# Kernel optimization log

Hardware: AMD Instinct MI355X
Metric: run time of the kernel (lower is better)

Reference implementation:

```python
import jax, jax.numpy as jnp
import numpy as np

N = 32768      # nodes
DIN = 256      # in_channels (space dim; hyperbolic input has DIN+1 dims)
DOUT = 256     # out_channels
H = 8          # num_heads
K = 1.0        # Lorentz curvature manifold.k
P = 2          # power_k
EPS = 1e-6


def _lorentz(key, n, d):
    # random point on Lorentz manifold: time = sqrt(||space||^2 + k)
    s = jax.random.normal(key, (n, d), jnp.float32)
    t = jnp.sqrt(jnp.sum(s * s, -1, keepdims=True) + K)
    return jnp.concatenate([t, s], -1)


def setup_inputs() -> dict:
    key = jax.random.key(0)
    ks = jax.random.split(key, 8)
    sc = 0.02
    return {
        "query_input": _lorentz(ks[0], N, DIN),
        "source_input": _lorentz(ks[1], N, DIN),
        "Wq_w": jax.random.normal(ks[2], (H, DOUT, DIN + 1), jnp.float32) * sc,
        "Wq_b": jnp.zeros((H, DOUT), jnp.float32),
        "Wk_w": jax.random.normal(ks[3], (H, DOUT, DIN + 1), jnp.float32) * sc,
        "Wk_b": jnp.zeros((H, DOUT), jnp.float32),
        "Wv_w": jax.random.normal(ks[4], (H, DOUT, DIN + 1), jnp.float32) * sc,
        "Wv_b": jnp.zeros((H, DOUT), jnp.float32),
        "norm_scale": jnp.ones((), jnp.float32),
        "v_map_w": jax.random.normal(ks[5], (DOUT, DIN), jnp.float32) * sc,
        "v_map_b": jnp.zeros((DOUT,), jnp.float32),
        "final_w": jax.random.normal(ks[6], (DOUT, H * DOUT), jnp.float32) * sc,
        "final_b": jnp.zeros((DOUT,), jnp.float32),
    }


def _hyp_linear(x, W, b):
    # HypLinear for all heads at once. x: [N, Din+1], W: [H, Dout, Din+1], b: [H, Dout]
    xs = jnp.einsum('ni,hoi->nho', x, W) + b              # space part [N,H,Dout]
    xt = jnp.sqrt(jnp.sum(xs * xs, -1, keepdims=True) + K)  # Lorentz time
    return jnp.concatenate([xt, xs], -1)                  # [N,H,Dout+1]


def _fp(x, p=P):
    # fp(x) = ||x|| / ||x^p|| * x^p  (per-vector rescaled power map)
    norm_x = jnp.linalg.norm(x, axis=-1, keepdims=True)
    xp = x ** p
    norm_xp = jnp.linalg.norm(xp, axis=-1, keepdims=True)
    return norm_x / norm_xp * xp


def reference(query_input, source_input, Wq_w, Wq_b, Wk_w, Wk_b, Wv_w, Wv_b,
              norm_scale, v_map_w, v_map_b, final_w, final_b):
    q = _hyp_linear(query_input, Wq_w, Wq_b)    # [N,H,D+1]
    k = _hyp_linear(source_input, Wk_w, Wk_b)   # [N,H,D+1]
    v = _hyp_linear(source_input, Wv_w, Wv_b)   # [N,H,D+1]

    # linear_focus_attention: drop time dim
    qs, ks_, vs = q[..., 1:], k[..., 1:], v[..., 1:]     # [N,H,D]
    dscale = jnp.abs(norm_scale) + EPS
    phi_q = _fp((jax.nn.relu(qs) + EPS) / dscale)
    phi_k = _fp((jax.nn.relu(ks_) + EPS) / dscale)

    ktv = jnp.einsum('nhm,nhd->hmd', phi_k, vs)          # [H,D,D]
    numerator = jnp.einsum('nhm,hmd->nhd', phi_q, ktv)   # [N,H,D]
    denominator = jnp.einsum('nhd,hd->nh', phi_q, jnp.sum(phi_k, 0))[..., None]
    attn = numerator / (denominator + EPS)

    vss = vs @ v_map_w.T + v_map_b                       # v_map_mlp(v)
    attn = attn + vss

    # trans_heads_concat -> final_linear
    out = attn.reshape(N, H * DOUT) @ final_w.T + final_b  # [N,Dout]

    # lift back to Lorentz manifold
    t = jnp.sqrt(jnp.sum(out * out, -1, keepdims=True) + K)
    return jnp.concatenate([t, out], -1)                 # [N,Dout+1]
```

## Files before the change

kernel.cpp:

```cpp
#include <hip/hip_runtime.h>
#include <hip/hip_bf16.h>


#define EPSF 1e-6f

typedef __attribute__((ext_vector_type(8))) short bf16x8;
typedef __attribute__((ext_vector_type(8))) unsigned short u16x8;
typedef __attribute__((ext_vector_type(4))) float f32x4;
typedef float f32x4a __attribute__((ext_vector_type(4), aligned(4)));

__device__ __forceinline__ float b2f(unsigned short u) {
    union { unsigned int i; float f; } c;
    c.i = ((unsigned int)u) << 16;
    return c.f;
}
__device__ __forceinline__ unsigned short f2b(float f) {
    __hip_bfloat16 h = __float2bfloat16(f);
    union { __hip_bfloat16 h; unsigned short u; } c;
    c.h = h;
    return c.u;
}

__global__ void zero_kernel(float* __restrict__ p, int n) {
    int i = blockIdx.x * 256 + threadIdx.x;
    if (i < n) p[i] = 0.f;
}

__global__ __launch_bounds__(256) void wconv_kernel(
    const float* __restrict__ Wq, const float* __restrict__ Wk, const float* __restrict__ Wv,
    const float* __restrict__ Bq, const float* __restrict__ Bk, const float* __restrict__ Bv,
    unsigned short* __restrict__ Wbf, float* __restrict__ biasAll)
{
    const int t = threadIdx.x;
    const int b = blockIdx.x;
    if (b < 6144) {
        const int mat = b >> 11, lr = b & 2047;
        const float* Ws = (mat == 0 ? Wq : mat == 1 ? Wk : Wv) + (size_t)lr * 257;
        Wbf[(size_t)b * 288 + t] = f2b(Ws[t]);
        if (t < 32) {
            float v = (t == 0) ? Ws[256] : 0.f;
            Wbf[(size_t)b * 288 + 256 + t] = f2b(v);
        }
    } else {
        const int e = (b - 6144) * 256 + t;
        const int mat = e >> 11, r = e & 2047;
        biasAll[e] = (mat == 0 ? Bq : mat == 1 ? Bk : Bv)[r];
    }
}

__global__ __launch_bounds__(256) void w2g_kernel(
    const float* __restrict__ vmw,
    const float* __restrict__ fw,
    float* __restrict__ G32)
{
    const int t = threadIdx.x;
    const int h = blockIdx.x >> 3;
    const int i0 = (blockIdx.x & 7) * 32;

    __shared__ __align__(16) float xlds[16][40];
    __shared__ float wlds[256][17];

    float acc[32];
#pragma unroll
    for (int r = 0; r < 32; ++r) acc[r] = 0.f;

    const int ar = t >> 3;
    const int ak = (t & 7) * 2;
    const int wk = t & 15;
    const int wo = (t >> 4) * 16;

    for (int d0 = 0; d0 < 256; d0 += 16) {
        xlds[ak][ar]     = vmw[(size_t)(d0 + ak) * 256 + i0 + ar];
        xlds[ak + 1][ar] = vmw[(size_t)(d0 + ak + 1) * 256 + i0 + ar];
#pragma unroll
        for (int j = 0; j < 16; ++j)
            wlds[wo + j][wk] = fw[(size_t)(wo + j) * 2048 + h * 256 + d0 + wk];
        __syncthreads();
#pragma unroll
        for (int kk = 0; kk < 16; ++kk) {
            float bv = wlds[t][kk];
            const float4* xr = (const float4*)(&xlds[kk][0]);
#pragma unroll
            for (int g = 0; g < 8; ++g) {
                float4 xv = xr[g];
                acc[g * 4 + 0] = fmaf(xv.x, bv, acc[g * 4 + 0]);
                acc[g * 4 + 1] = fmaf(xv.y, bv, acc[g * 4 + 1]);
                acc[g * 4 + 2] = fmaf(xv.z, bv, acc[g * 4 + 2]);
                acc[g * 4 + 3] = fmaf(xv.w, bv, acc[g * 4 + 3]);
            }
        }
        __syncthreads();
    }
#pragma unroll
    for (int r = 0; r < 32; ++r)
        G32[(size_t)t * 2048 + h * 256 + i0 + r] = acc[r];
}

__global__ __launch_bounds__(256) void bias2_kernel(
    const float* __restrict__ vmb, const float* __restrict__ fw,
    const float* __restrict__ fb, const float* __restrict__ Bv,
    const float* __restrict__ G32, float* __restrict__ bias2)
{
    const int o = blockIdx.x;
    const int t = threadIdx.x;
    float s = 0.f, sb = 0.f;
#pragma unroll
    for (int i = 0; i < 8; ++i) {
        const int j = t + i * 256;
        s += fw[(size_t)o * 2048 + j];
        sb += Bv[j] * G32[(size_t)o * 2048 + j];
    }
    s = s * vmb[t] + sb;
#pragma unroll
    for (int off = 32; off > 0; off >>= 1) s += __shfl_down(s, off, 64);
    __shared__ float r4[4];
    if ((t & 63) == 0) r4[t >> 6] = s;
    __syncthreads();
    if (t == 0) bias2[o] = fb[o] + r4[0] + r4[1] + r4[2] + r4[3];
}

__global__ __launch_bounds__(256) void gm_kernel(
    const float* __restrict__ Wv, const float* __restrict__ G32,
    float* __restrict__ Mf32)
{
    __shared__ float Gt[64][33];
    __shared__ float Wt[32][33];
    const int t = threadIdx.x;
    const int o0 = blockIdx.x * 64, i0 = blockIdx.y * 32, k0 = blockIdx.z * 256;
    const int ii = t & 31, og = t >> 5;
    float acc[8] = {};
    for (int kk0 = k0; kk0 < k0 + 256; kk0 += 32) {
#pragma unroll
        for (int r = 0; r < 8; ++r) {
            const int e = t + r * 256;
            Gt[e >> 5][e & 31] = G32[(size_t)(o0 + (e >> 5)) * 2048 + kk0 + (e & 31)];
        }
#pragma unroll
        for (int r = 0; r < 4; ++r) {
            const int e = t + r * 256;
            const int kk = e >> 5, i = i0 + (e & 31);
            Wt[kk][e & 31] = (i < 257) ? Wv[(size_t)(kk0 + kk) * 257 + i] : 0.f;
        }
        __syncthreads();
#pragma unroll
        for (int kk = 0; kk < 32; ++kk) {
            float wv_ = Wt[kk][ii];
#pragma unroll
            for (int r = 0; r < 8; ++r)
                acc[r] = fmaf(Gt[og * 8 + r][kk], wv_, acc[r]);
        }
        __syncthreads();
    }
#pragma unroll
    for (int r = 0; r < 8; ++r)
        atomicAdd(&Mf32[(size_t)(o0 + og * 8 + r) * 288 + i0 + ii], acc[r]);
}

__global__ void gmcvt_kernel(const float* __restrict__ Mf32, unsigned short* __restrict__ Mbf) {
    const int i = blockIdx.x * 256 + threadIdx.x;
    Mbf[i] = f2b(Mf32[i]);
}

__device__ __forceinline__ void stage_load(
    const float* __restrict__ XA, const unsigned short* __restrict__ WB, int k,
    f32x4a& cx0, f32x4a& cx1, u16x8 cw[4])
{
    cx0 = *(const f32x4a*)(XA + k);
    cx1 = *(const f32x4a*)(XA + k + 4);
#pragma unroll
    for (int qq = 0; qq < 4; ++qq)
        cw[qq] = *(const u16x8*)(WB + (size_t)qq * 64 * 288 + k);
}

__device__ __forceinline__ void stage_write(
    unsigned short* __restrict__ la, unsigned short* __restrict__ lb,
    int ar, int akg, f32x4a cx0, f32x4a cx1, const u16x8 cw[4])
{
    u16x8 pk;
    pk[0] = f2b(cx0[0]); pk[1] = f2b(cx0[1]); pk[2] = f2b(cx0[2]); pk[3] = f2b(cx0[3]);
    pk[4] = f2b(cx1[0]); pk[5] = f2b(cx1[1]); pk[6] = f2b(cx1[2]); pk[7] = f2b(cx1[3]);
    *(u16x8*)(&la[ar * 40 + akg]) = pk;
#pragma unroll
    for (int qq = 0; qq < 4; ++qq)
        *(u16x8*)(&lb[(ar + qq * 64) * 40 + akg]) = cw[qq];
}

__device__ __forceinline__ void tstore(
    unsigned short* __restrict__ smem, const f32x4 acc[4][4],
    unsigned short* __restrict__ outT, int cbase, int m0, int CH,
    int wn, int l15, int q, int t)
{
#pragma unroll
    for (int i = 0; i < 4; ++i)
#pragma unroll
        for (int j = 0; j < 4; ++j) {
            const int cl = wn + j * 16 + l15;
#pragma unroll
            for (int r2 = 0; r2 < 4; r2 += 2) {
                const int nl = i * 16 + q * 4 + r2;
                const unsigned int pk =
                    (unsigned int)f2b(acc[i][j][r2]) |
                    ((unsigned int)f2b(acc[i][j][r2 + 1]) << 16);
                *(unsigned int*)(&smem[cl * 64 + (((nl >> 3) ^ (cl & 7)) << 3) + (nl & 7)]) = pk;
            }
        }
    __syncthreads();
#pragma unroll
    for (int k = 0; k < 8; ++k) {
        const int task = k * 256 + t;
        const int cl = task >> 3, nq = task & 7;
        *(u16x8*)(outT + (size_t)(cbase + cl) * CH + m0 + nq * 8) =
            *(const u16x8*)(&smem[cl * 64 + ((nq ^ (cl & 7)) << 3)]);
    }
}

__global__ __launch_bounds__(256, 3) void proj_all(
    int pass,
    const float* __restrict__ X,
    const unsigned short* __restrict__ Wbf,
    const unsigned short* __restrict__ Mbf,
    const float* __restrict__ biasAll,
    unsigned short* __restrict__ phiOut,
    unsigned short* __restrict__ vsOut,
    float* __restrict__ xOut,
    const float* __restrict__ nsc,
    const float* __restrict__ colsum_in,
    float* __restrict__ colrep,
    int CH)
{
    __shared__ __align__(16) unsigned short smem[27008];
    float* reds2 = (float*)(smem + 25600);
    float* reds4 = reds2 + 256;
    float* rowv  = reds4 + 256;
    float* rowx  = rowv + 64;

    const int t = threadIdx.x;
    const int m0 = blockIdx.x * 64;
    const int y  = blockIdx.y;
    const int lane = t & 63, w = t >> 6;
    const int wn = w * 64;
    const int l15 = lane & 15, q = lane >> 4;
    const int ar = t >> 2, akg = (t & 3) * 8;

    int mode, hcol;
    const unsigned short* Wb;
    const float* bb;
    if (pass == 1)   { mode = 3; hcol = y * 256; Wb = Wbf + (size_t)hcol * 288;          bb = biasAll + hcol; }
    else if (y < 8)  { mode = 0; hcol = y * 256; Wb = Wbf + (size_t)(2048 + hcol) * 288; bb = biasAll + 2048 + hcol; }
    else if (y < 16) { mode = 1; hcol = (y - 8) * 256; Wb = Wbf + (size_t)(4096 + hcol) * 288; bb = biasAll + 4096 + hcol; }
    else             { mode = 2; hcol = 0; Wb = Mbf; bb = nullptr; }

    const float* XA = X + (size_t)(m0 + ar) * 257 + akg;
    const unsigned short* WB = Wb + (size_t)ar * 288 + akg;

    f32x4 acc[4][4] = {};
    f32x4a cx0, cx1;
    u16x8 cw[4];

    stage_load(XA, WB, 0, cx0, cx1, cw);
    stage_write(smem, smem + 5120, ar, akg, cx0, cx1, cw);
    stage_load(XA, WB, 32, cx0, cx1, cw);
    __syncthreads();

#pragma unroll
    for (int ks = 0; ks < 8; ++ks) {
        const int b = ks & 1;
        unsigned short* la = smem + (b ? 2560 : 0);
        unsigned short* lb = smem + (b ? 15360 : 5120);
        bf16x8 af[4], bfr[4];
#pragma unroll
        for (int i = 0; i < 4; ++i)
            af[i] = *(const bf16x8*)(&la[(i * 16 + l15) * 40 + q * 8]);
#pragma unroll
        for (int j = 0; j < 4; ++j)
            bfr[j] = *(const bf16x8*)(&lb[(wn + j * 16 + l15) * 40 + q * 8]);
#pragma unroll
        for (int i = 0; i < 4; ++i)
#pragma unroll
            for (int j = 0; j < 4; ++j)
                acc[i][j] = __builtin_amdgcn_mfma_f32_16x16x32_bf16(af[i], bfr[j], acc[i][j], 0, 0, 0);
        if (ks < 7) {
            unsigned short* la2 = smem + (b ? 0 : 2560);
            unsigned short* lb2 = smem + (b ? 5120 : 15360);
            stage_write(la2, lb2, ar, akg, cx0, cx1, cw);
            if (ks < 6) stage_load(XA, WB, (ks + 2) * 32, cx0, cx1, cw);
        }
        __syncthreads();
    }

    if (t < 64) rowx[t] = b2f(f2b(X[(size_t)(m0 + t) * 257 + 256]));
    __syncthreads();

    {
        float w256[4];
#pragma unroll
        for (int j = 0; j < 4; ++j)
            w256[j] = b2f(Wb[(size_t)(wn + j * 16 + l15) * 288 + 256]);
#pragma unroll
        for (int i = 0; i < 4; ++i)
#pragma unroll
            for (int r = 0; r < 4; ++r) {
                const float xv = rowx[i * 16 + q * 4 + r];
#pragma unroll
                for (int j = 0; j < 4; ++j)
                    acc[i][j][r] += xv * w256[j];
            }
    }

    if (mode == 2) {
#pragma unroll
        for (int j = 0; j < 4; ++j) {
            const int cg = wn + j * 16 + l15;
#pragma unroll
            for (int i = 0; i < 4; ++i)
#pragma unroll
                for (int r = 0; r < 4; ++r) {
                    const int n = m0 + i * 16 + q * 4 + r;
                    xOut[(size_t)n * 257 + 1 + cg] = acc[i][j][r];
                }
        }
        return;
    }
    if (mode == 1) {
#pragma unroll
        for (int j = 0; j < 4; ++j) {
            const float bias = bb[wn + j * 16 + l15];
#pragma unroll
            for (int i = 0; i < 4; ++i)
#pragma unroll
                for (int r = 0; r < 4; ++r)
                    acc[i][j][r] += bias;
        }
        tstore(smem, acc, vsOut, hcol, m0, CH, wn, l15, q, t);
        return;
    }

    const float c = fabsf(nsc[0]) + EPSF;
    float bias[4];
#pragma unroll
    for (int j = 0; j < 4; ++j) bias[j] = bb[wn + j * 16 + l15];

    float a2[4][4], a4[4][4];
#pragma unroll
    for (int i = 0; i < 4; ++i)
#pragma unroll
        for (int r = 0; r < 4; ++r) { a2[i][r] = 0.f; a4[i][r] = 0.f; }
#pragma unroll
    for (int i = 0; i < 4; ++i)
#pragma unroll
        for (int j = 0; j < 4; ++j)
#pragma unroll
            for (int r = 0; r < 4; ++r) {
                float uu = fmaxf(acc[i][j][r] + bias[j], 0.f) + EPSF;
                float q2 = uu * uu;
                acc[i][j][r] = q2;
                a2[i][r] += q2;
                a4[i][r] += q2 * q2;
            }
#pragma unroll
    for (int m = 1; m <= 8; m <<= 1) {
#pragma unroll
        for (int i = 0; i < 4; ++i)
#pragma unroll
            for (int r = 0; r < 4; ++r) {
                a2[i][r] += __shfl_xor(a2[i][r], m, 64);
                a4[i][r] += __shfl_xor(a4[i][r], m, 64);
            }
    }
    if (l15 == 0) {
#pragma unroll
        for (int i = 0; i < 4; ++i)
#pragma unroll
            for (int r = 0; r < 4; ++r) {
                reds2[w * 64 + i * 16 + q * 4 + r] = a2[i][r];
                reds4[w * 64 + i * 16 + q * 4 + r] = a4[i][r];
            }
    }
    __syncthreads();
    if (t < 64) {
        float s2t = reds2[t] + reds2[64 + t] + reds2[128 + t] + reds2[192 + t];
        float s4t = reds4[t] + reds4[64 + t] + reds4[128 + t] + reds4[192 + t];
        rowv[t] = sqrtf(s2t) / (c * sqrtf(s4t));
    }
    __syncthreads();
    float sc_[4][4];
#pragma unroll
    for (int i = 0; i < 4; ++i)
#pragma unroll
        for (int r = 0; r < 4; ++r) sc_[i][r] = rowv[i * 16 + q * 4 + r];

    if (mode == 0) {
        float colp[4];
#pragma unroll
        for (int j = 0; j < 4; ++j) colp[j] = 0.f;
#pragma unroll
        for (int i = 0; i < 4; ++i)
#pragma unroll
            for (int j = 0; j < 4; ++j)
#pragma unroll
                for (int r = 0; r < 4; ++r) {
                    float ph = acc[i][j][r] * sc_[i][r];
                    acc[i][j][r] = ph;
                    colp[j] += ph;
                }
        tstore(smem, acc, phiOut, hcol, m0, CH, wn, l15, q, t);
#pragma unroll
        for (int j = 0; j < 4; ++j) {
            colp[j] += __shfl_xor(colp[j], 16, 64);
            colp[j] += __shfl_xor(colp[j], 32, 64);
        }
        if (q == 0) {
            float* dst = colrep + (size_t)(blockIdx.x & 7) * 2048;
#pragma unroll
            for (int j = 0; j < 4; ++j)
                atomicAdd(&dst[hcol + wn + j * 16 + l15], colp[j]);
        }
    } else {
        float cs[4];
#pragma unroll
        for (int j = 0; j < 4; ++j) cs[j] = colsum_in[hcol + wn + j * 16 + l15];
        float dp[4][4];
#pragma unroll
        for (int i = 0; i < 4; ++i)
#pragma unroll
            for (int r = 0; r < 4; ++r) dp[i][r] = 0.f;
#pragma unroll
        for (int i = 0; i < 4; ++i)
#pragma unroll
            for (int j = 0; j < 4; ++j)
#pragma unroll
                for (int r = 0; r < 4; ++r) {
                    float ph = acc[i][j][r] * sc_[i][r];
                    acc[i][j][r] = ph;
                    dp[i][r] += ph * cs[j];
                }
#pragma unroll
        for (int m = 1; m <= 8; m <<= 1) {
#pragma unroll
            for (int i = 0; i < 4; ++i)
#pragma unroll
                for (int r = 0; r < 4; ++r)
                    dp[i][r] += __shfl_xor(dp[i][r], m, 64);
        }
        if (l15 == 0) {
#pragma unroll
            for (int i = 0; i < 4; ++i)
#pragma unroll
                for (int r = 0; r < 4; ++r)
                    reds2[w * 64 + i * 16 + q * 4 + r] = dp[i][r];
        }
        __syncthreads();
        if (t < 64) {
            float dt = reds2[t] + reds2[64 + t] + reds2[128 + t] + reds2[192 + t];
            rowv[t] = 1.f / (dt + EPSF);
        }
        __syncthreads();
#pragma unroll
        for (int i = 0; i < 4; ++i)
#pragma unroll
            for (int r = 0; r < 4; ++r) sc_[i][r] = rowv[i * 16 + q * 4 + r];
#pragma unroll
        for (int i = 0; i < 4; ++i)
#pragma unroll
            for (int j = 0; j < 4; ++j)
#pragma unroll
                for (int r = 0; r < 4; ++r) {
                    const int n = m0 + i * 16 + q * 4 + r;
                    phiOut[(size_t)n * 2048 + hcol + wn + j * 16 + l15] =
                        f2b(acc[i][j][r] * sc_[i][r]);
                }
    }
}

__global__ __launch_bounds__(256) void merge_colsum(
    const float* __restrict__ rep, float* __restrict__ out)
{
    const int cidx = blockIdx.x * 256 + threadIdx.x;
    float s = 0.f;
#pragma unroll
    for (int r = 0; r < 8; ++r) s += rep[(size_t)r * 2048 + cidx];
    out[cidx] = s;
}

__global__ __launch_bounds__(256) void ktv_mfma(
    const unsigned short* __restrict__ phiT,
    const unsigned short* __restrict__ vsT,
    float* __restrict__ ktv, int CH)
{
    __shared__ __align__(16) unsigned short lAT[128 * 64];
    __shared__ __align__(16) unsigned short lBT[128 * 64];
    const int t = threadIdx.x;
    const int h = blockIdx.y;
    const int split = blockIdx.x >> 2;
    const int tile = blockIdx.x & 3;
    const int m0 = (tile >> 1) * 128, d0 = (tile & 1) * 128;
    const int chh = h * 256;
    const int lane = t & 63, w = t >> 6;
    const int wm = (w >> 1) * 64, wn = (w & 1) * 64;
    const int l15 = lane & 15, q = lane >> 4;
    const int sl7 = l15 & 7;

    const int scg  = t >> 3;
    const int snq  = t & 7;
    const int sbase = scg * 64 + ((snq ^ (scg & 7)) << 3);

    f32x4 acc[4][4] = {};
    const int nb0 = split * 512;

    const unsigned short* pA = phiT + (size_t)(chh + m0 + scg) * CH + snq * 8;
    const unsigned short* pB = vsT  + (size_t)(chh + d0 + scg) * CH + snq * 8;

    u16x8 cA[4], cB[4], nA[4], nB[4];
#pragma unroll
    for (int k = 0; k < 4; ++k) {
        cA[k] = *(const u16x8*)(pA + (size_t)(k * 32) * CH + nb0);
        cB[k] = *(const u16x8*)(pB + (size_t)(k * 32) * CH + nb0);
    }

    for (int it = 0; it < 8; ++it) {
#pragma unroll
        for (int k = 0; k < 4; ++k) {
            *(u16x8*)(&lAT[k * 2048 + sbase]) = cA[k];
            *(u16x8*)(&lBT[k * 2048 + sbase]) = cB[k];
        }
        if (it < 7) {
            const int nb = nb0 + (it + 1) * 64;
#pragma unroll
            for (int k = 0; k < 4; ++k) {
                nA[k] = *(const u16x8*)(pA + (size_t)(k * 32) * CH + nb);
                nB[k] = *(const u16x8*)(pB + (size_t)(k * 32) * CH + nb);
            }
        }
        __syncthreads();
#pragma unroll
        for (int sub = 0; sub < 2; ++sub) {
            const int slot = ((sub * 4 + q) ^ sl7) << 3;
            bf16x8 af[4], bfr[4];
#pragma unroll
            for (int i = 0; i < 4; ++i)
                af[i] = *(const bf16x8*)(&lAT[(wm + i * 16 + l15) * 64 + slot]);
#pragma unroll
            for (int j = 0; j < 4; ++j)
                bfr[j] = *(const bf16x8*)(&lBT[(wn + j * 16 + l15) * 64 + slot]);
#pragma unroll
            for (int i = 0; i < 4; ++i)
#pragma unroll
                for (int j = 0; j < 4; ++j)
                    acc[i][j] = __builtin_amdgcn_mfma_f32_16x16x32_bf16(af[i], bfr[j], acc[i][j], 0, 0, 0);
        }
        __syncthreads();
        if (it < 7) {
#pragma unroll
            for (int k = 0; k < 4; ++k) { cA[k] = nA[k]; cB[k] = nB[k]; }
        }
    }
#pragma unroll
    for (int i = 0; i < 4; ++i)
#pragma unroll
        for (int j = 0; j < 4; ++j)
#pragma unroll
            for (int r = 0; r < 4; ++r) {
                const int m = m0 + wm + i * 16 + q * 4 + r;
                const int d = d0 + wn + j * 16 + l15;
                atomicAdd(&ktv[((size_t)chh + m) * 256 + d], acc[i][j][r]);
            }
}

__device__ __forceinline__ void fin_load(
    const unsigned short* __restrict__ Abuf, const unsigned short* __restrict__ W2T,
    int n0, int d0, int t, int k0,
    u16x8& A0, u16x8& A1, u16x8& B)
{
    {
        const int row = t >> 2, kg = (t & 3) * 8;
        A0 = *(const u16x8*)(Abuf + (size_t)(n0 + row) * 2048 + ((k0 + kg) & 2047));
    }
    {
        const int e = t + 256;
        const int row = e >> 2, kg = (e & 3) * 8;
        A1 = *(const u16x8*)(Abuf + (size_t)(n0 + row) * 2048 + ((k0 + kg) & 2047));
    }
    {
        const int row = t >> 2, kg = (t & 3) * 8;
        B = *(const u16x8*)(W2T + (size_t)(d0 + row) * 4096 + k0 + kg);
    }
}

__global__ __launch_bounds__(256) void final_mfma(
    const unsigned short* __restrict__ Abuf,
    const unsigned short* __restrict__ W2T,
    int kbeg, int kend,
    float* __restrict__ outp)
{
    __shared__ __align__(16) unsigned short smem[15360];
    const int t = threadIdx.x;
    const int n0 = blockIdx.x * 128;
    const int d0 = blockIdx.y * 64;
    const int ksp = (kend - kbeg) / gridDim.z;
    const int kb = kbeg + blockIdx.z * ksp;
    const int lane = t & 63, w = t >> 6;
    const int wm = w * 32;
    const int l15 = lane & 15, q = lane >> 4;
    const int row = t >> 2, kg = (t & 3) * 8;
    const int row2 = (t + 256) >> 2;

    f32x4 acc[2][4] = {};
    u16x8 cA0, cA1, cB;
    fin_load(Abuf, W2T, n0, d0, t, kb, cA0, cA1, cB);
    {
        *(u16x8*)(&smem[row * 40 + kg]) = cA0;
        *(u16x8*)(&smem[10240 + row * 40 + kg]) = cB;
        *(u16x8*)(&smem[row2 * 40 + kg]) = cA1;
    }
    const int nst = ksp >> 5;
    if (nst > 1) fin_load(Abuf, W2T, n0, d0, t, kb + 32, cA0, cA1, cB);
    __syncthreads();

    for (int s = 0; s < nst; ++s) {
        const int b = s & 1;
        unsigned short* la = smem + (b ? 5120 : 0);
        unsigned short* lb = smem + (b ? 12800 : 10240);
        bf16x8 af[2], bfr[4];
#pragma unroll
        for (int i = 0; i < 2; ++i)
            af[i] = *(const bf16x8*)(&la[(wm + i * 16 + l15) * 40 + q * 8]);
#pragma unroll
        for (int j = 0; j < 4; ++j)
            bfr[j] = *(const bf16x8*)(&lb[(j * 16 + l15) * 40 + q * 8]);
#pragma unroll
        for (int i = 0; i < 2; ++i)
#pragma unroll
            for (int j = 0; j < 4; ++j)
                acc[i][j] = __builtin_amdgcn_mfma_f32_16x16x32_bf16(af[i], bfr[j], acc[i][j], 0, 0, 0);
        if (s + 1 < nst) {
            unsigned short* la2 = smem + (b ? 0 : 5120);
            unsigned short* lb2 = smem + (b ? 10240 : 12800);
            *(u16x8*)(&la2[row * 40 + kg]) = cA0;
            *(u16x8*)(&lb2[row * 40 + kg]) = cB;
            *(u16x8*)(&la2[row2 * 40 + kg]) = cA1;
            if (s + 2 < nst)
                fin_load(Abuf, W2T, n0, d0, t, kb + (s + 2) * 32, cA0, cA1, cB);
        }
        __syncthreads();
    }
#pragma unroll
    for (int i = 0; i < 2; ++i)
#pragma unroll
        for (int j = 0; j < 4; ++j)
#pragma unroll
            for (int r = 0; r < 4; ++r) {
                const int n = n0 + wm + i * 16 + q * 4 + r;
                const int d = d0 + j * 16 + l15;
                atomicAdd(&outp[(size_t)n * 257 + 1 + d], acc[i][j][r]);
            }
}

__global__ __launch_bounds__(256) void w2u_kernel(
    const float* __restrict__ ktv,
    const float* __restrict__ fw,
    unsigned short* __restrict__ W2T)
{
    const int t = threadIdx.x;
    const int h = blockIdx.x >> 3;
    const int m0 = (blockIdx.x & 7) * 32;

    __shared__ __align__(16) float xlds[16][40];
    __shared__ float wlds[256][17];

    float acc[32];
#pragma unroll
    for (int r = 0; r < 32; ++r) acc[r] = 0.f;

    const int ar = t >> 3;
    const int ak = (t & 7) * 2;
    const int wk = t & 15;
    const int wo = (t >> 4) * 16;

    for (int d0 = 0; d0 < 256; d0 += 16) {
        {
            const float* src = ktv + (size_t)(h * 256 + m0 + ar) * 256 + d0 + ak;
            xlds[ak][ar]     = src[0];
            xlds[ak + 1][ar] = src[1];
        }
#pragma unroll
        for (int j = 0; j < 16; ++j)
            wlds[wo + j][wk] = fw[(size_t)(wo + j) * 2048 + h * 256 + d0 + wk];
        __syncthreads();
#pragma unroll
        for (int kk = 0; kk < 16; ++kk) {
            float bv = wlds[t][kk];
            const float4* xr = (const float4*)(&xlds[kk][0]);
#pragma unroll
            for (int g = 0; g < 8; ++g) {
                float4 xv = xr[g];
                acc[g * 4 + 0] = fmaf(xv.x, bv, acc[g * 4 + 0]);
                acc[g * 4 + 1] = fmaf(xv.y, bv, acc[g * 4 + 1]);
                acc[g * 4 + 2] = fmaf(xv.z, bv, acc[g * 4 + 2]);
                acc[g * 4 + 3] = fmaf(xv.w, bv, acc[g * 4 + 3]);
            }
        }
        __syncthreads();
    }
#pragma unroll
    for (int r = 0; r < 32; ++r)
        W2T[(size_t)t * 4096 + h * 256 + m0 + r] = f2b(acc[r]);
}

__global__ __launch_bounds__(256) void lift_kernel(
    const float* __restrict__ bias2, float* __restrict__ outp)
{
    const int t = threadIdx.x;
    const int lane = t & 63;
    const int w = t >> 6;
    const int n0 = blockIdx.x * 64 + w * 16;
    float b[4];
#pragma unroll
    for (int j = 0; j < 4; ++j) b[j] = bias2[lane + j * 64];
    for (int r = 0; r < 16; ++r) {
        float* row = outp + (size_t)(n0 + r) * 257;
        float v[4];
        float s = 0.f;
#pragma unroll
        for (int j = 0; j < 4; ++j) {
            v[j] = row[1 + lane + j * 64] + b[j];
            s = fmaf(v[j], v[j], s);
        }
#pragma unroll
        for (int off = 32; off > 0; off >>= 1) s += __shfl_down(s, off, 64);
#pragma unroll
        for (int j = 0; j < 4; ++j) row[1 + lane + j * 64] = v[j];
        if (lane == 0) row[0] = sqrtf(s + 1.0f);
    }
}

extern "C" void kernel_launch(void* const* d_in, const int* in_sizes, int n_in,
                              void* d_out, int out_size, void* d_ws, size_t ws_size,
                              hipStream_t stream)
{
    const float* xq  = (const float*)d_in[0];
    const float* xs  = (const float*)d_in[1];
    const float* Wq  = (const float*)d_in[2];
    const float* Bq  = (const float*)d_in[3];
    const float* Wk  = (const float*)d_in[4];
    const float* Bk  = (const float*)d_in[5];
    const float* Wv  = (const float*)d_in[6];
    const float* Bv  = (const float*)d_in[7];
    const float* nsc = (const float*)d_in[8];
    const float* vmw = (const float*)d_in[9];
    const float* vmb = (const float*)d_in[10];
    const float* fw  = (const float*)d_in[11];
    const float* fb  = (const float*)d_in[12];
    float* outp = (float*)d_out;

    char* ws = (char*)d_ws;
    float* ktv          = (float*)(ws + 0);
    float* colrep       = (float*)(ws + 2097152);
    float* Mf32         = (float*)(ws + 2162688);
    float* colsum       = (float*)(ws + 2457600);
    float* bias2        = (float*)(ws + 2465792);
    float* biasAll      = (float*)(ws + 2466816);
    unsigned short* W2T = (unsigned short*)(ws + 2491392);
    unsigned short* Wbf = (unsigned short*)(ws + 4588544);
    float* G32          = (float*)(ws + 8127488);
    unsigned short* Mbf = (unsigned short*)(ws + 10224640);
    const size_t fixedBytes = 10372096;

    int CH = 2048;
    if (ws_size >= fixedBytes + (size_t)8192 * 8192) CH = 8192;
    else if (ws_size >= fixedBytes + (size_t)4096 * 8192) CH = 4096;
    const int NCHK = 32768 / CH;
    unsigned short* phibuf = (unsigned short*)(ws + fixedBytes);
    unsigned short* vsT    = (unsigned short*)(ws + fixedBytes + (size_t)CH * 4096);

    zero_kernel<<<dim3(2400), 256, 0, stream>>>(ktv, 614400);
    wconv_kernel<<<dim3(6168), 256, 0, stream>>>(Wq, Wk, Wv, Bq, Bk, Bv, Wbf, biasAll);
    w2g_kernel<<<dim3(64), 256, 0, stream>>>(vmw, fw, G32);
    bias2_kernel<<<dim3(256), 256, 0, stream>>>(vmb, fw, fb, Bv, G32, bias2);
    gm_kernel<<<dim3(4, 9, 8), 256, 0, stream>>>(Wv, G32, Mf32);
    gmcvt_kernel<<<dim3(288), 256, 0, stream>>>(Mf32, Mbf);

    for (int c = 0; c < NCHK; ++c) {
        const float* xs_c = xs + (size_t)c * CH * 257;
        float* out_c = outp + (size_t)c * CH * 257;
        proj_all<<<dim3(CH / 64, 17), 256, 0, stream>>>(
            0, xs_c, Wbf, Mbf, biasAll, phibuf, vsT, out_c,
            nsc, nullptr, colrep, CH);
        ktv_mfma<<<dim3((CH / 512) * 4, 8), 256, 0, stream>>>(phibuf, vsT, ktv, CH);
    }

    merge_colsum<<<dim3(8), 256, 0, stream>>>(colrep, colsum);
    w2u_kernel<<<dim3(64), 256, 0, stream>>>(ktv, fw, W2T);

    for (int c = 0; c < NCHK; ++c) {
        const float* xq_c = xq + (size_t)c * CH * 257;
        float* out_c = outp + (size_t)c * CH * 257;
        proj_all<<<dim3(CH / 64, 8), 256, 0, stream>>>(
            1, xq_c, Wbf, Mbf, biasAll, phibuf, vsT, out_c,
            nsc, colsum, nullptr, CH);
        final_mfma<<<dim3(CH / 128, 4, 4), 256, 0, stream>>>(phibuf, W2T, 0, 2048, out_c);
    }

    lift_kernel<<<dim3(512), 256, 0, stream>>>(bias2, outp);
}
```

Before: 1.166 ms.

## Stripe phi/vs layout, single-buffer LDS, coalesced pass-1 stores, larger chunks

Stores phi and vs transposes in per-64-row stripes so the ktv kernel reads contiguous 2048-element blocks instead of rows strided by CH. Drops the double-buffered LDS in proj_all and final_mfma for single buffers with register prefetch, which lowers LDS use but adds a sync per step. Pass-1 phi output now goes through LDS for coalesced row stores. Allows CH up to 32768 to cut launches, and halves the final_mfma k-split to reduce atomics. Losing LDS double buffering may expose more load latency.

```diff
diff --git a/kernel.cpp b/kernel.cpp
--- a/kernel.cpp
+++ b/kernel.cpp
@@ -8,6 +8,8 @@
 typedef __attribute__((ext_vector_type(8))) unsigned short u16x8;
 typedef __attribute__((ext_vector_type(4))) float f32x4;
 typedef float f32x4a __attribute__((ext_vector_type(4), aligned(4)));
+
+#define STRIPE 131072
 
 __device__ __forceinline__ float b2f(unsigned short u) {
     union { unsigned int i; float f; } c;
@@ -161,60 +163,7 @@
     Mbf[i] = f2b(Mf32[i]);
 }
 
-__device__ __forceinline__ void stage_load(
-    const float* __restrict__ XA, const unsigned short* __restrict__ WB, int k,
-    f32x4a& cx0, f32x4a& cx1, u16x8 cw[4])
-{
-    cx0 = *(const f32x4a*)(XA + k);
-    cx1 = *(const f32x4a*)(XA + k + 4);
-#pragma unroll
-    for (int qq = 0; qq < 4; ++qq)
-        cw[qq] = *(const u16x8*)(WB + (size_t)qq * 64 * 288 + k);
-}
-
-__device__ __forceinline__ void stage_write(
-    unsigned short* __restrict__ la, unsigned short* __restrict__ lb,
-    int ar, int akg, f32x4a cx0, f32x4a cx1, const u16x8 cw[4])
-{
-    u16x8 pk;
-    pk[0] = f2b(cx0[0]); pk[1] = f2b(cx0[1]); pk[2] = f2b(cx0[2]); pk[3] = f2b(cx0[3]);
-    pk[4] = f2b(cx1[0]); pk[5] = f2b(cx1[1]); pk[6] = f2b(cx1[2]); pk[7] = f2b(cx1[3]);
-    *(u16x8*)(&la[ar * 40 + akg]) = pk;
-#pragma unroll
-    for (int qq = 0; qq < 4; ++qq)
-        *(u16x8*)(&lb[(ar + qq * 64) * 40 + akg]) = cw[qq];
-}
-
-__device__ __forceinline__ void tstore(
-    unsigned short* __restrict__ smem, const f32x4 acc[4][4],
-    unsigned short* __restrict__ outT, int cbase, int m0, int CH,
-    int wn, int l15, int q, int t)
-{
-#pragma unroll
-    for (int i = 0; i < 4; ++i)
-#pragma unroll
-        for (int j = 0; j < 4; ++j) {
-            const int cl = wn + j * 16 + l15;
-#pragma unroll
-            for (int r2 = 0; r2 < 4; r2 += 2) {
-                const int nl = i * 16 + q * 4 + r2;
-                const unsigned int pk =
-                    (unsigned int)f2b(acc[i][j][r2]) |
-                    ((unsigned int)f2b(acc[i][j][r2 + 1]) << 16);
-                *(unsigned int*)(&smem[cl * 64 + (((nl >> 3) ^ (cl & 7)) << 3) + (nl & 7)]) = pk;
-            }
-        }
-    __syncthreads();
-#pragma unroll
-    for (int k = 0; k < 8; ++k) {
-        const int task = k * 256 + t;
-        const int cl = task >> 3, nq = task & 7;
-        *(u16x8*)(outT + (size_t)(cbase + cl) * CH + m0 + nq * 8) =
-            *(const u16x8*)(&smem[cl * 64 + ((nq ^ (cl & 7)) << 3)]);
-    }
-}
-
-__global__ __launch_bounds__(256, 3) void proj_all(
+__global__ __launch_bounds__(256) void proj_all(
     int pass,
     const float* __restrict__ X,
     const unsigned short* __restrict__ Wbf,
@@ -228,11 +177,13 @@
     float* __restrict__ colrep,
     int CH)
 {
-    __shared__ __align__(16) unsigned short smem[27008];
-    float* reds2 = (float*)(smem + 25600);
-    float* reds4 = reds2 + 256;
-    float* rowv  = reds4 + 256;
-    float* rowx  = rowv + 64;
+    __shared__ __align__(16) unsigned short smem[16896];
+    __shared__ float reds2[4][64];
+    __shared__ float reds4[4][64];
+    __shared__ float rowv[64];
+    __shared__ float rowx[64];
+    unsigned short* lA = smem;
+    unsigned short* lB = smem + 64 * 40;
 
     const int t = threadIdx.x;
     const int m0 = blockIdx.x * 64;
@@ -245,46 +196,56 @@
     int mode, hcol;
     const unsigned short* Wb;
     const float* bb;
-    if (pass == 1)   { mode = 3; hcol = y * 256; Wb = Wbf + (size_t)hcol * 288;          bb = biasAll + hcol; }
-    else if (y < 8)  { mode = 0; hcol = y * 256; Wb = Wbf + (size_t)(2048 + hcol) * 288; bb = biasAll + 2048 + hcol; }
+    if (pass == 1)   { mode = 3; hcol = y * 256; Wb = Wbf + (size_t)hcol * 288;                bb = biasAll + hcol; }
+    else if (y < 8)  { mode = 0; hcol = y * 256; Wb = Wbf + (size_t)(2048 + hcol) * 288;       bb = biasAll + 2048 + hcol; }
     else if (y < 16) { mode = 1; hcol = (y - 8) * 256; Wb = Wbf + (size_t)(4096 + hcol) * 288; bb = biasAll + 4096 + hcol; }
     else             { mode = 2; hcol = 0; Wb = Mbf; bb = nullptr; }
 
+    f32x4 acc[4][4] = {};
     const float* XA = X + (size_t)(m0 + ar) * 257 + akg;
     const unsigned short* WB = Wb + (size_t)ar * 288 + akg;
 
-    f32x4 acc[4][4] = {};
     f32x4a cx0, cx1;
     u16x8 cw[4];
-
-    stage_load(XA, WB, 0, cx0, cx1, cw);
-    stage_write(smem, smem + 5120, ar, akg, cx0, cx1, cw);
-    stage_load(XA, WB, 32, cx0, cx1, cw);
-    __syncthreads();
-
-#pragma unroll
+    cx0 = *(const f32x4a*)(XA);
+    cx1 = *(const f32x4a*)(XA + 4);
+#pragma unroll
+    for (int qq = 0; qq < 4; ++qq)
+        cw[qq] = *(const u16x8*)(WB + (size_t)qq * 64 * 288);
+
     for (int ks = 0; ks < 8; ++ks) {
-        const int b = ks & 1;
-        unsigned short* la = smem + (b ? 2560 : 0);
-        unsigned short* lb = smem + (b ? 15360 : 5120);
+        {
+            u16x8 pk;
+            pk[0] = f2b(cx0[0]); pk[1] = f2b(cx0[1]);
+            pk[2] = f2b(cx0[2]); pk[3] = f2b(cx0[3]);
+            pk[4] = f2b(cx1[0]); pk[5] = f2b(cx1[1]);
+            pk[6] = f2b(cx1[2]); pk[7] = f2b(cx1[3]);
+            *(u16x8*)(&lA[ar * 40 + akg]) = pk;
+        }
+#pragma unroll
+        for (int qq = 0; qq < 4; ++qq)
+            *(u16x8*)(&lB[(ar + qq * 64) * 40 + akg]) = cw[qq];
+        if (ks < 7) {
+            const int k1 = (ks + 1) * 32;
+            cx0 = *(const f32x4a*)(XA + k1);
+            cx1 = *(const f32x4a*)(XA + k1 + 4);
+#pragma unroll
+            for (int qq = 0; qq < 4; ++qq)
+                cw[qq] = *(const u16x8*)(WB + (size_t)qq * 64 * 288 + k1);
+        }
+        __syncthreads();
         bf16x8 af[4], bfr[4];
 #pragma unroll
         for (int i = 0; i < 4; ++i)
-            af[i] = *(const bf16x8*)(&la[(i * 16 + l15) * 40 + q * 8]);
+            af[i] = *(const bf16x8*)(&lA[(i * 16 + l15) * 40 + q * 8]);
 #pragma unroll
         for (int j = 0; j < 4; ++j)
-            bfr[j] = *(const bf16x8*)(&lb[(wn + j * 16 + l15) * 40 + q * 8]);
+            bfr[j] = *(const bf16x8*)(&lB[(wn + j * 16 + l15) * 40 + q * 8]);
 #pragma unroll
         for (int i = 0; i < 4; ++i)
 #pragma unroll
             for (int j = 0; j < 4; ++j)
                 acc[i][j] = __builtin_amdgcn_mfma_f32_16x16x32_bf16(af[i], bfr[j], acc[i][j], 0, 0, 0);
-        if (ks < 7) {
-            unsigned short* la2 = smem + (b ? 0 : 2560);
-            unsigned short* lb2 = smem + (b ? 5120 : 15360);
-            stage_write(la2, lb2, ar, akg, cx0, cx1, cw);
-            if (ks < 6) stage_load(XA, WB, (ks + 2) * 32, cx0, cx1, cw);
-        }
         __syncthreads();
     }
 
@@ -321,6 +282,7 @@
         }
         return;
     }
+
     if (mode == 1) {
 #pragma unroll
         for (int j = 0; j < 4; ++j) {
@@ -331,7 +293,29 @@
                 for (int r = 0; r < 4; ++r)
                     acc[i][j][r] += bias;
         }
-        tstore(smem, acc, vsOut, hcol, m0, CH, wn, l15, q, t);
+#pragma unroll
+        for (int i = 0; i < 4; ++i)
+#pragma unroll
+            for (int j = 0; j < 4; ++j) {
+                const int cl = wn + j * 16 + l15;
+#pragma unroll
+                for (int r2 = 0; r2 < 4; r2 += 2) {
+                    const int nl = i * 16 + q * 4 + r2;
+                    const unsigned int pk =
+                        (unsigned int)f2b(acc[i][j][r2]) |
+                        ((unsigned int)f2b(acc[i][j][r2 + 1]) << 16);
+                    *(unsigned int*)(&smem[cl * 64 + (((nl >> 3) ^ (cl & 7)) << 3) + (nl & 7)]) = pk;
+                }
+            }
+        __syncthreads();
+#pragma unroll
+        for (int k = 0; k < 8; ++k) {
+            const int task = k * 256 + t;
+            const int cl = task >> 3, nq = task & 7;
+            *(u16x8*)(vsOut + (size_t)blockIdx.x * STRIPE +
+                      (size_t)(hcol + cl) * 64 + nq * 8) =
+                *(const u16x8*)(&smem[cl * 64 + ((nq ^ (cl & 7)) << 3)]);
+        }
         return;
     }
 
@@ -372,14 +356,14 @@
         for (int i = 0; i < 4; ++i)
 #pragma unroll
             for (int r = 0; r < 4; ++r) {
-                reds2[w * 64 + i * 16 + q * 4 + r] = a2[i][r];
-                reds4[w * 64 + i * 16 + q * 4 + r] = a4[i][r];
+                reds2[w][i * 16 + q * 4 + r] = a2[i][r];
+                reds4[w][i * 16 + q * 4 + r] = a4[i][r];
             }
     }
     __syncthreads();
     if (t < 64) {
-        float s2t = reds2[t] + reds2[64 + t] + reds2[128 + t] + reds2[192 + t];
-        float s4t = reds4[t] + reds4[64 + t] + reds4[128 + t] + reds4[192 + t];
+        float s2t = reds2[0][t] + reds2[1][t] + reds2[2][t] + reds2[3][t];
+        float s4t = reds4[0][t] + reds4[1][t] + reds4[2][t] + reds4[3][t];
         rowv[t] = sqrtf(s2t) / (c * sqrtf(s4t));
     }
     __syncthreads();
@@ -403,7 +387,29 @@
                     acc[i][j][r] = ph;
                     colp[j] += ph;
                 }
-        tstore(smem, acc, phiOut, hcol, m0, CH, wn, l15, q, t);
+#pragma unroll
+        for (int i = 0; i < 4; ++i)
+#pragma unroll
+            for (int j = 0; j < 4; ++j) {
+                const int cl = wn + j * 16 + l15;
+#pragma unroll
+                for (int r2 = 0; r2 < 4; r2 += 2) {
+                    const int nl = i * 16 + q * 4 + r2;
+                    const unsigned int pk =
+                        (unsigned int)f2b(acc[i][j][r2]) |
+                        ((unsigned int)f2b(acc[i][j][r2 + 1]) << 16);
+                    *(unsigned int*)(&smem[cl * 64 + (((nl >> 3) ^ (cl & 7)) << 3) + (nl & 7)]) = pk;
+                }
+            }
+        __syncthreads();
+#pragma unroll
+        for (int k = 0; k < 8; ++k) {
+            const int task = k * 256 + t;
+            const int cl = task >> 3, nq = task & 7;
+            *(u16x8*)(phiOut + (size_t)blockIdx.x * STRIPE +
+                      (size_t)(hcol + cl) * 64 + nq * 8) =
+                *(const u16x8*)(&smem[cl * 64 + ((nq ^ (cl & 7)) << 3)]);
+        }
 #pragma unroll
         for (int j = 0; j < 4; ++j) {
             colp[j] += __shfl_xor(colp[j], 16, 64);
@@ -447,11 +453,11 @@
             for (int i = 0; i < 4; ++i)
 #pragma unroll
                 for (int r = 0; r < 4; ++r)
-                    reds2[w * 64 + i * 16 + q * 4 + r] = dp[i][r];
+                    reds2[w][i * 16 + q * 4 + r] = dp[i][r];
         }
         __syncthreads();
         if (t < 64) {
-            float dt = reds2[t] + reds2[64 + t] + reds2[128 + t] + reds2[192 + t];
+            float dt = reds2[0][t] + reds2[1][t] + reds2[2][t] + reds2[3][t];
             rowv[t] = 1.f / (dt + EPSF);
         }
         __syncthreads();
@@ -462,13 +468,22 @@
 #pragma unroll
         for (int i = 0; i < 4; ++i)
 #pragma unroll
-            for (int j = 0; j < 4; ++j)
+            for (int j = 0; j < 4; ++j) {
+                const int cl = wn + j * 16 + l15;
 #pragma unroll
                 for (int r = 0; r < 4; ++r) {
-                    const int n = m0 + i * 16 + q * 4 + r;
-                    phiOut[(size_t)n * 2048 + hcol + wn + j * 16 + l15] =
-                        f2b(acc[i][j][r] * sc_[i][r]);
+                    const int nl = i * 16 + q * 4 + r;
+                    smem[nl * 264 + cl] = f2b(acc[i][j][r] * sc_[i][r]);
                 }
+            }
+        __syncthreads();
+#pragma unroll
+        for (int k = 0; k < 8; ++k) {
+            const int task = k * 256 + t;
+            const int rowl = task >> 5, ck = (task & 31) * 8;
+            *(u16x8*)(phiOut + (size_t)(m0 + rowl) * 2048 + hcol + ck) =
+                *(const u16x8*)(&smem[rowl * 264 + ck]);
+        }
     }
 }
 
@@ -505,16 +520,16 @@
     const int sbase = scg * 64 + ((snq ^ (scg & 7)) << 3);
 
     f32x4 acc[4][4] = {};
-    const int nb0 = split * 512;
-
-    const unsigned short* pA = phiT + (size_t)(chh + m0 + scg) * CH + snq * 8;
-    const unsigned short* pB = vsT  + (size_t)(chh + d0 + scg) * CH + snq * 8;
+    const int st0 = split * 8;
+
+    const unsigned short* pA = phiT + (size_t)(chh + m0 + scg) * 64 + snq * 8;
+    const unsigned short* pB = vsT  + (size_t)(chh + d0 + scg) * 64 + snq * 8;
 
     u16x8 cA[4], cB[4], nA[4], nB[4];
 #pragma unroll
     for (int k = 0; k < 4; ++k) {
-        cA[k] = *(const u16x8*)(pA + (size_t)(k * 32) * CH + nb0);
-        cB[k] = *(const u16x8*)(pB + (size_t)(k * 32) * CH + nb0);
+        cA[k] = *(const u16x8*)(pA + (size_t)st0 * STRIPE + k * 2048);
+        cB[k] = *(const u16x8*)(pB + (size_t)st0 * STRIPE + k * 2048);
     }
 
     for (int it = 0; it < 8; ++it) {
@@ -524,11 +539,11 @@
             *(u16x8*)(&lBT[k * 2048 + sbase]) = cB[k];
         }
         if (it < 7) {
-            const int nb = nb0 + (it + 1) * 64;
+            const size_t so = (size_t)(st0 + it + 1) * STRIPE;
 #pragma unroll
             for (int k = 0; k < 4; ++k) {
-                nA[k] = *(const u16x8*)(pA + (size_t)(k * 32) * CH + nb);
-                nB[k] = *(const u16x8*)(pB + (size_t)(k * 32) * CH + nb);
+                nA[k] = *(const u16x8*)(pA + so + k * 2048);
+                nB[k] = *(const u16x8*)(pB + so + k * 2048);
             }
         }
         __syncthreads();
@@ -592,56 +607,50 @@
     int kbeg, int kend,
     float* __restrict__ outp)
 {
-    __shared__ __align__(16) unsigned short smem[15360];
+    __shared__ __align__(16) unsigned short lA[128 * 40];
+    __shared__ __align__(16) unsigned short lB[64 * 40];
     const int t = threadIdx.x;
     const int n0 = blockIdx.x * 128;
     const int d0 = blockIdx.y * 64;
-    const int ksp = (kend - kbeg) / gridDim.z;
-    const int kb = kbeg + blockIdx.z * ksp;
+    const int khalf = (kend - kbeg) >> 1;
+    const int kb = kbeg + blockIdx.z * khalf;
+    const int ke = kb + khalf;
     const int lane = t & 63, w = t >> 6;
     const int wm = w * 32;
     const int l15 = lane & 15, q = lane >> 4;
-    const int row = t >> 2, kg = (t & 3) * 8;
-    const int row2 = (t + 256) >> 2;
 
     f32x4 acc[2][4] = {};
-    u16x8 cA0, cA1, cB;
+    u16x8 cA0, cA1, cB, nA0, nA1, nB;
     fin_load(Abuf, W2T, n0, d0, t, kb, cA0, cA1, cB);
-    {
-        *(u16x8*)(&smem[row * 40 + kg]) = cA0;
-        *(u16x8*)(&smem[10240 + row * 40 + kg]) = cB;
-        *(u16x8*)(&smem[row2 * 40 + kg]) = cA1;
-    }
-    const int nst = ksp >> 5;
-    if (nst > 1) fin_load(Abuf, W2T, n0, d0, t, kb + 32, cA0, cA1, cB);
-    __syncthreads();
-
-    for (int s = 0; s < nst; ++s) {
-        const int b = s & 1;
-        unsigned short* la = smem + (b ? 5120 : 0);
-        unsigned short* lb = smem + (b ? 12800 : 10240);
+
+    for (int k0 = kb; k0 < ke; k0 += 32) {
+        {
+            const int row = t >> 2, kg = (t & 3) * 8;
+            *(u16x8*)(&lA[row * 40 + kg]) = cA0;
+            *(u16x8*)(&lB[row * 40 + kg]) = cB;
+        }
+        {
+            const int e = t + 256;
+            const int row = e >> 2, kg = (e & 3) * 8;
+            *(u16x8*)(&lA[row * 40 + kg]) = cA1;
+        }
+        if (k0 + 32 < ke)
+            fin_load(Abuf, W2T, n0, d0, t, k0 + 32, nA0, nA1, nB);
+        __syncthreads();
         bf16x8 af[2], bfr[4];
 #pragma unroll
         for (int i = 0; i < 2; ++i)
-            af[i] = *(const bf16x8*)(&la[(wm + i * 16 + l15) * 40 + q * 8]);
+            af[i] = *(const bf16x8*)(&lA[(wm + i * 16 + l15) * 40 + q * 8]);
 #pragma unroll
         for (int j = 0; j < 4; ++j)
-            bfr[j] = *(const bf16x8*)(&lb[(j * 16 + l15) * 40 + q * 8]);
+            bfr[j] = *(const bf16x8*)(&lB[(j * 16 + l15) * 40 + q * 8]);
 #pragma unroll
         for (int i = 0; i < 2; ++i)
 #pragma unroll
             for (int j = 0; j < 4; ++j)
                 acc[i][j] = __builtin_amdgcn_mfma_f32_16x16x32_bf16(af[i], bfr[j], acc[i][j], 0, 0, 0);
-        if (s + 1 < nst) {
-            unsigned short* la2 = smem + (b ? 0 : 5120);
-            unsigned short* lb2 = smem + (b ? 10240 : 12800);
-            *(u16x8*)(&la2[row * 40 + kg]) = cA0;
-            *(u16x8*)(&lb2[row * 40 + kg]) = cB;
-            *(u16x8*)(&la2[row2 * 40 + kg]) = cA1;
-            if (s + 2 < nst)
-                fin_load(Abuf, W2T, n0, d0, t, kb + (s + 2) * 32, cA0, cA1, cB);
-        }
-        __syncthreads();
+        __syncthreads();
+        if (k0 + 32 < ke) { cA0 = nA0; cA1 = nA1; cB = nB; }
     }
 #pragma unroll
     for (int i = 0; i < 2; ++i)
@@ -766,8 +775,10 @@
     const size_t fixedBytes = 10372096;
 
     int CH = 2048;
-    if (ws_size >= fixedBytes + (size_t)8192 * 8192) CH = 8192;
-    else if (ws_size >= fixedBytes + (size_t)4096 * 8192) CH = 4096;
+    if      (ws_size >= fixedBytes + (size_t)32768 * 8192) CH = 32768;
+    else if (ws_size >= fixedBytes + (size_t)16384 * 8192) CH = 16384;
+    else if (ws_size >= fixedBytes + (size_t)8192 * 8192)  CH = 8192;
+    else if (ws_size >= fixedBytes + (size_t)4096 * 8192)  CH = 4096;
     const int NCHK = 32768 / CH;
     unsigned short* phibuf = (unsigned short*)(ws + fixedBytes);
     unsigned short* vsT    = (unsigned short*)(ws + fixedBytes + (size_t)CH * 4096);
@@ -797,7 +808,7 @@
         proj_all<<<dim3(CH / 64, 8), 256, 0, stream>>>(
             1, xq_c, Wbf, Mbf, biasAll, phibuf, vsT, out_c,
             nsc, colsum, nullptr, CH);
-        final_mfma<<<dim3(CH / 128, 4, 4), 256, 0, stream>>>(phibuf, W2T, 0, 2048, out_c);
+        final_mfma<<<dim3(CH / 128, 4, 2), 256, 0, stream>>>(phibuf, W2T, 0, 2048, out_c);
     }
 
     lift_kernel<<<dim3(512), 256, 0, stream>>>(bias2, outp);
```

Result: faster. 1.049 ms (-10.0%).
